# Optimization experiments

Hardware: AMD Instinct MI355X
Metric: run time of the kernel (lower is better)

The kernel has to match this reference:

```python
import jax, jax.numpy as jnp
import numpy as np
from jax import lax

REG_STRENGTH = 0.01
TEMPERATURE = 0.1


def _pav_nonincreasing(y):
    """Pool-adjacent-violators for isotonic L2 regression with a
    nonincreasing constraint (matches torchsort's isotonic_l2).
    Returns (solution [n], block_id [n])."""
    n = y.shape[0]

    def body(carry, yi):
        m, c, t = carry  # block means, block counts, stack top
        m = m.at[t].set(yi)
        c = c.at[t].set(1)

        def cond(st):
            m_, c_, t_ = st
            return (t_ > 0) & (m_[t_ - 1] < m_[t_])

        def merge(st):
            m_, c_, t_ = st
            tot = m_[t_ - 1] * c_[t_ - 1] + m_[t_] * c_[t_]
            cc = c_[t_ - 1] + c_[t_]
            m_ = m_.at[t_ - 1].set(tot / cc)
            c_ = c_.at[t_ - 1].set(cc).at[t_].set(0)
            return (m_, c_, t_ - 1)

        m, c, t = lax.while_loop(cond, merge, (m, c, t))
        return (m, c, t + 1), None

    init = (jnp.zeros(n, y.dtype), jnp.zeros(n, jnp.int32), jnp.int32(0))
    (m, c, _), _ = lax.scan(body, init, y)
    sol = jnp.repeat(m, c, total_repeat_length=n)
    blk = jnp.repeat(jnp.arange(n), c, total_repeat_length=n)
    return sol, blk


@jax.custom_vjp
def _isotonic_l2(y):
    return _pav_nonincreasing(y)[0]


def _iso_fwd(y):
    sol, blk = _pav_nonincreasing(y)
    return sol, blk


def _iso_bwd(blk, g):
    n = g.shape[0]
    sums = jax.ops.segment_sum(g, blk, num_segments=n)
    cnts = jax.ops.segment_sum(jnp.ones_like(g), blk, num_segments=n)
    return ((sums / jnp.maximum(cnts, 1.0))[blk],)


_isotonic_l2.defvjp(_iso_fwd, _iso_bwd)


def soft_sort_ascending(scores, reg_strength):
    """torchsort.soft_sort with L2 regularization. scores: [B, R]."""
    n = scores.shape[-1]
    w = jnp.arange(n, 0, -1, dtype=scores.dtype) / reg_strength  # [n, ..., 1]/rs
    perm = jnp.argsort(scores, axis=-1)
    s = -jnp.take_along_axis(scores, perm, axis=-1)  # descending sort of -scores
    sol = jax.vmap(_isotonic_l2)(w[None, :] - s)
    return sol - w  # ascending soft-sorted values, [B, R]


def setup_inputs() -> dict:
    key = jax.random.key(0)
    k1, k2 = jax.random.split(key)
    scores = jax.random.normal(k1, (128, 8192), dtype=jnp.float32)
    ref_class = jax.random.randint(k2, (8192,), 0, 10, dtype=jnp.int32)
    return {"scores": scores, "ref_class": ref_class, "k": 32, "K": 8}


def reference(scores, ref_class, k, K):
    B, R = scores.shape
    rc = ref_class
    if rc.ndim == 1:
        rc = jnp.broadcast_to(rc[None, :], (B, R))
    rc = rc.astype(scores.dtype)
    sorted_vals = soft_sort_ascending(scores, REG_STRENGTH)  # [B, R]
    yk = sorted_vals[:, -k:]                                  # top-k largest, [B, k]
    M = jnp.abs(scores[:, None, :] - yk[:, :, None])          # [B, k, R]
    soft_mask = jax.nn.softmax(-M / TEMPERATURE, axis=-1)     # [B, k, R]
    soft_label_expectation = jnp.einsum('bkr,br->bk', soft_mask, rc)
    return yk, soft_label_expectation
```

## Files before the change

### kernel.cpp

```cpp
#include <hip/hip_runtime.h>
#include <math.h>

#define R_N    8192
#define K_TOP  32
#define SLAB   128
#define C1     14.426950408889634f
#define NEG_BIG (-3.0e38f)

__device__ __forceinline__ float fast_exp2(float x) {
#if __has_builtin(__builtin_amdgcn_exp2f)
    return __builtin_amdgcn_exp2f(x);
#else
    return exp2f(x);
#endif
}

__device__ __forceinline__ float merge_asc32(float v, int l) {
#pragma unroll
    for (int j = 16; j > 0; j >>= 1) {
        float pv = __shfl_xor(v, j, 64);
        v = ((l & j) == 0) ? fminf(v, pv) : fmaxf(v, pv);
    }
    return v;
}

__device__ __forceinline__ float merge_asc64(float v, int lane) {
#pragma unroll
    for (int j = 32; j > 0; j >>= 1) {
        float pv = __shfl_xor(v, j, 64);
        v = ((lane & j) == 0) ? fminf(v, pv) : fmaxf(v, pv);
    }
    return v;
}

__device__ __forceinline__ float sort64_asc(float v, int lane) {
#pragma unroll
    for (int k = 2; k <= 64; k <<= 1) {
#pragma unroll
        for (int j = k >> 1; j > 0; j >>= 1) {
            float pv = __shfl_xor(v, j, 64);
            bool keep_min = (((lane & k) == 0) == ((lane & j) == 0));
            v = keep_min ? fminf(v, pv) : fmaxf(v, pv);
        }
    }
    return v;
}

extern "C" __global__ void __launch_bounds__(1024)
k_fused(const float* __restrict__ scores, const int* __restrict__ rc,
        float* __restrict__ out, int B) {
    __shared__ float    slab[16 * SLAB];
    __shared__ float    lists[16 * 32];
    __shared__ float    dsS[32], dsC[32];
    __shared__ float    pbuf[32];
    __shared__ unsigned dcnt;

    const int row  = blockIdx.x;
    const int tid  = threadIdx.x;
    const int lane = tid & 63;
    const int la   = tid & 31;
    const int half = (tid >> 5) & 1;
    const int wv   = tid >> 6;

    const float4* s4 = (const float4*)(scores + (size_t)row * R_N);
    const int4*   c4 = (const int4*)rc;
    float4 sa = s4[tid], sb = s4[tid + 1024];
    int4   ca = c4[tid], cb = c4[tid + 1024];
    float se[8] = {sa.x, sa.y, sa.z, sa.w, sb.x, sb.y, sb.z, sb.w};
    float ce[8] = {(float)ca.x, (float)ca.y, (float)ca.z, (float)ca.w,
                   (float)cb.x, (float)cb.y, (float)cb.z, (float)cb.w};

    if (tid == 0) dcnt = 0;

    float ex[8];
#pragma unroll
    for (int e = 0; e < 8; ++e) ex[e] = fast_exp2(C1 * se[e]);

    float tmax = se[0];
#pragma unroll
    for (int e = 1; e < 8; ++e) tmax = fmaxf(tmax, se[e]);
    float srt = sort64_asc(tmax, lane);
    float t_w = __shfl(srt, 32, 64);

    slab[wv * SLAB + lane]      = NEG_BIG;
    slab[wv * SLAB + 64 + lane] = NEG_BIG;
    const unsigned long long ltm = (1ull << lane) - 1ull;
    unsigned base = 0;
#pragma unroll
    for (int e = 0; e < 8; ++e) {
        unsigned long long mm = __ballot(se[e] >= t_w);
        if (se[e] >= t_w) {
            unsigned idx = base + (unsigned)__popcll(mm & ltm);
            if (idx < SLAB) slab[wv * SLAB + idx] = se[e];
        }
        base += (unsigned)__popcll(mm);
    }
    __asm__ volatile("s_waitcnt lgkmcnt(0)" ::: "memory");

    float r0 = slab[wv * SLAB + lane];
    float r1 = slab[wv * SLAB + 64 + lane];
    r0 = sort64_asc(r0, lane);
    r1 = sort64_asc(r1, lane);
    float hi = fmaxf(r0, __shfl_xor(r1, 63, 64));
    hi = merge_asc64(hi, lane);
    if (lane >= 32) lists[wv * 32 + (lane - 32)] = hi;
    __syncthreads();

    float v0 = lists[(8 * half + 0) * 32 + la];
    float v1 = lists[(8 * half + 1) * 32 + la];
    float v2 = lists[(8 * half + 2) * 32 + la];
    float v3 = lists[(8 * half + 3) * 32 + la];
    float v4 = lists[(8 * half + 4) * 32 + la];
    float v5 = lists[(8 * half + 5) * 32 + la];
    float v6 = lists[(8 * half + 6) * 32 + la];
    float v7 = lists[(8 * half + 7) * 32 + la];
    v0 = merge_asc32(fmaxf(v0, __shfl_xor(v1, 31, 64)), la);
    v2 = merge_asc32(fmaxf(v2, __shfl_xor(v3, 31, 64)), la);
    v4 = merge_asc32(fmaxf(v4, __shfl_xor(v5, 31, 64)), la);
    v6 = merge_asc32(fmaxf(v6, __shfl_xor(v7, 31, 64)), la);
    v0 = merge_asc32(fmaxf(v0, __shfl_xor(v2, 31, 64)), la);
    v4 = merge_asc32(fmaxf(v4, __shfl_xor(v6, 31, 64)), la);
    v0 = merge_asc32(fmaxf(v0, __shfl_xor(v4, 31, 64)), la);
    float fin = merge_asc32(fmaxf(v0, __shfl_xor(v0, 63, 64)), la);

    if (tid < 32) out[(size_t)row * K_TOP + tid] = fin;
    const float y0 = __shfl(fin, 0, 64);

    float P = 0.f, Pc = 0.f;
#pragma unroll
    for (int e = 0; e < 8; ++e) {
        if (se[e] <= y0) {
            P += ex[e];
            Pc = fmaf(ce[e], ex[e], Pc);
        } else {
            unsigned idx = atomicAdd(&dcnt, 1u);
            dsS[idx] = se[e];
            dsC[idx] = ce[e];
        }
    }
#pragma unroll
    for (int off = 32; off > 0; off >>= 1) {
        P  += __shfl_xor(P,  off, 64);
        Pc += __shfl_xor(Pc, off, 64);
    }
    if (lane == 0) { pbuf[wv * 2] = P; pbuf[wv * 2 + 1] = Pc; }
    __syncthreads();
    float Pt = 0.f, Pct = 0.f;
#pragma unroll
    for (int w = 0; w < 16; ++w) { Pt += pbuf[w * 2]; Pct += pbuf[w * 2 + 1]; }
    const int nD = (int)dcnt;

    const int   j  = 2 * wv + half;
    const float yj = __shfl(fin, j, 64);
    float d = 0.f, n = 0.f;
    if (la < nD) {
        float s = dsS[la], c = dsC[la];
        float e_ = fast_exp2(-C1 * fabsf(s - yj));
        d = e_;
        n = c * e_;
    }
#pragma unroll
    for (int off = 16; off > 0; off >>= 1) {
        d += __shfl_xor(d, off, 64);
        n += __shfl_xor(n, off, 64);
    }
    if (la == 0) {
        float e0 = fast_exp2(-C1 * yj);
        out[(size_t)B * K_TOP + (size_t)row * K_TOP + j] =
            fmaf(Pct, e0, n) / fmaf(Pt, e0, d);
    }
}

extern "C" void kernel_launch(void* const* d_in, const int* in_sizes, int n_in,
                              void* d_out, int out_size, void* d_ws, size_t ws_size,
                              hipStream_t stream) {
    const float* scores = (const float*)d_in[0];
    const int*   rc     = (const int*)d_in[1];
    const int R = in_sizes[1];
    const int B = in_sizes[0] / R;
    float* out = (float*)d_out;

    hipLaunchKernelGGL(k_fused, dim3(B), dim3(1024), 0, stream, scores, rc, out, B);
}
```

Measured before the change: 68.32 us.

## Split each row across two blocks with a finalize kernel and packed class bits

Splits each row's work across two 512-thread blocks (2B blocks instead of B) that each compute a local top-32 and exp sums in double precision, then a small second kernel merges the two halves and computes the soft-label expectation. The reference class is packed into the low 4 mantissa bits of each score so the class travels with the value, and the sums over all elements are computed unconditionally and then corrected by subtracting the top elements. The second slab sort is skipped when few candidates exist. This adds a second launch and a global workspace round-trip, perturbs scores slightly through bit packing, and relies on class ids fitting in 4 bits.

```diff
diff --git a/kernel.cpp b/kernel.cpp
--- a/kernel.cpp
+++ b/kernel.cpp
@@ -1,11 +1,11 @@
 #include <hip/hip_runtime.h>
 #include <math.h>
 
-#define R_N    8192
-#define K_TOP  32
-#define SLAB   128
-#define C1     14.426950408889634f
-#define NEG_BIG (-3.0e38f)
+#define R_N       8192
+#define K_TOP     32
+#define WS_STRIDE 48
+#define C1        14.426950408889634f
+#define NEG_BIG   (-3.0e38f)
 
 __device__ __forceinline__ float fast_exp2(float x) {
 #if __has_builtin(__builtin_amdgcn_exp2f)
@@ -46,128 +46,151 @@
     return v;
 }
 
-extern "C" __global__ void __launch_bounds__(1024)
-k_fused(const float* __restrict__ scores, const int* __restrict__ rc,
-        float* __restrict__ out, int B) {
-    __shared__ float    slab[16 * SLAB];
-    __shared__ float    lists[16 * 32];
-    __shared__ float    dsS[32], dsC[32];
-    __shared__ float    pbuf[32];
-    __shared__ unsigned dcnt;
-
-    const int row  = blockIdx.x;
+extern "C" __global__ void __launch_bounds__(512)
+k_part(const float* __restrict__ scores, const int* __restrict__ rc,
+       float* __restrict__ ws) {
+    __shared__ float  slab[8 * 128];
+    __shared__ float  lists[8 * 32];
+    __shared__ double pb[8], pcb[8];
+
     const int tid  = threadIdx.x;
     const int lane = tid & 63;
-    const int la   = tid & 31;
-    const int half = (tid >> 5) & 1;
     const int wv   = tid >> 6;
-
-    const float4* s4 = (const float4*)(scores + (size_t)row * R_N);
-    const int4*   c4 = (const int4*)rc;
-    float4 sa = s4[tid], sb = s4[tid + 1024];
-    int4   ca = c4[tid], cb = c4[tid + 1024];
-    float se[8] = {sa.x, sa.y, sa.z, sa.w, sb.x, sb.y, sb.z, sb.w};
-    float ce[8] = {(float)ca.x, (float)ca.y, (float)ca.z, (float)ca.w,
-                   (float)cb.x, (float)cb.y, (float)cb.z, (float)cb.w};
-
-    if (tid == 0) dcnt = 0;
-
-    float ex[8];
-#pragma unroll
-    for (int e = 0; e < 8; ++e) ex[e] = fast_exp2(C1 * se[e]);
-
-    float tmax = se[0];
-#pragma unroll
-    for (int e = 1; e < 8; ++e) tmax = fmaxf(tmax, se[e]);
-    float srt = sort64_asc(tmax, lane);
-    float t_w = __shfl(srt, 32, 64);
-
-    slab[wv * SLAB + lane]      = NEG_BIG;
-    slab[wv * SLAB + 64 + lane] = NEG_BIG;
+    const int row  = blockIdx.x >> 1;
+    const int half = blockIdx.x & 1;
+
+    const float4* s4 = (const float4*)(scores + (size_t)row * R_N) + half * 1024;
+    const int4*   c4 = (const int4*)rc + half * 1024;
+    float4 sa = s4[tid], sb = s4[tid + 512];
+    int4   ca = c4[tid], cb = c4[tid + 512];
+    float sp[8];
+    {
+        float tf[8] = {sa.x, sa.y, sa.z, sa.w, sb.x, sb.y, sb.z, sb.w};
+        int   ci[8] = {ca.x, ca.y, ca.z, ca.w, cb.x, cb.y, cb.z, cb.w};
+#pragma unroll
+        for (int e = 0; e < 8; ++e) {
+            unsigned u = (__float_as_uint(tf[e]) & ~15u) | (unsigned)ci[e];
+            sp[e] = __uint_as_float(u);
+        }
+    }
+
+    double P = 0.0, Pc = 0.0;
+#pragma unroll
+    for (int e = 0; e < 8; ++e) {
+        float ex  = fast_exp2(C1 * sp[e]);
+        float cls = (float)(__float_as_uint(sp[e]) & 15u);
+        P  += (double)ex;
+        Pc += (double)(cls * ex);
+    }
+
+    float tmax = sp[0];
+#pragma unroll
+    for (int e = 1; e < 8; ++e) tmax = fmaxf(tmax, sp[e]);
+    float t_w = __shfl(sort64_asc(tmax, lane), 32, 64);
+
+    slab[wv * 128 + lane]      = NEG_BIG;
+    slab[wv * 128 + 64 + lane] = NEG_BIG;
     const unsigned long long ltm = (1ull << lane) - 1ull;
-    unsigned base = 0;
+    unsigned tot = 0;
 #pragma unroll
     for (int e = 0; e < 8; ++e) {
-        unsigned long long mm = __ballot(se[e] >= t_w);
-        if (se[e] >= t_w) {
-            unsigned idx = base + (unsigned)__popcll(mm & ltm);
-            if (idx < SLAB) slab[wv * SLAB + idx] = se[e];
-        }
-        base += (unsigned)__popcll(mm);
+        unsigned long long mm = __ballot(sp[e] >= t_w);
+        if (sp[e] >= t_w) {
+            unsigned idx = tot + (unsigned)__popcll(mm & ltm);
+            if (idx < 128) slab[wv * 128 + idx] = sp[e];
+        }
+        tot += (unsigned)__popcll(mm);
     }
     __asm__ volatile("s_waitcnt lgkmcnt(0)" ::: "memory");
 
-    float r0 = slab[wv * SLAB + lane];
-    float r1 = slab[wv * SLAB + 64 + lane];
-    r0 = sort64_asc(r0, lane);
-    r1 = sort64_asc(r1, lane);
-    float hi = fmaxf(r0, __shfl_xor(r1, 63, 64));
-    hi = merge_asc64(hi, lane);
+    float r0 = sort64_asc(slab[wv * 128 + lane], lane);
+    float hi;
+    if (tot > 64) {
+        float r1 = sort64_asc(slab[wv * 128 + 64 + lane], lane);
+        hi = merge_asc64(fmaxf(r0, __shfl_xor(r1, 63, 64)), lane);
+    } else {
+        hi = r0;
+    }
     if (lane >= 32) lists[wv * 32 + (lane - 32)] = hi;
-    __syncthreads();
-
-    float v0 = lists[(8 * half + 0) * 32 + la];
-    float v1 = lists[(8 * half + 1) * 32 + la];
-    float v2 = lists[(8 * half + 2) * 32 + la];
-    float v3 = lists[(8 * half + 3) * 32 + la];
-    float v4 = lists[(8 * half + 4) * 32 + la];
-    float v5 = lists[(8 * half + 5) * 32 + la];
-    float v6 = lists[(8 * half + 6) * 32 + la];
-    float v7 = lists[(8 * half + 7) * 32 + la];
-    v0 = merge_asc32(fmaxf(v0, __shfl_xor(v1, 31, 64)), la);
-    v2 = merge_asc32(fmaxf(v2, __shfl_xor(v3, 31, 64)), la);
-    v4 = merge_asc32(fmaxf(v4, __shfl_xor(v5, 31, 64)), la);
-    v6 = merge_asc32(fmaxf(v6, __shfl_xor(v7, 31, 64)), la);
-    v0 = merge_asc32(fmaxf(v0, __shfl_xor(v2, 31, 64)), la);
-    v4 = merge_asc32(fmaxf(v4, __shfl_xor(v6, 31, 64)), la);
-    v0 = merge_asc32(fmaxf(v0, __shfl_xor(v4, 31, 64)), la);
-    float fin = merge_asc32(fmaxf(v0, __shfl_xor(v0, 63, 64)), la);
-
-    if (tid < 32) out[(size_t)row * K_TOP + tid] = fin;
-    const float y0 = __shfl(fin, 0, 64);
-
-    float P = 0.f, Pc = 0.f;
-#pragma unroll
-    for (int e = 0; e < 8; ++e) {
-        if (se[e] <= y0) {
-            P += ex[e];
-            Pc = fmaf(ce[e], ex[e], Pc);
-        } else {
-            unsigned idx = atomicAdd(&dcnt, 1u);
-            dsS[idx] = se[e];
-            dsC[idx] = ce[e];
-        }
-    }
+
 #pragma unroll
     for (int off = 32; off > 0; off >>= 1) {
         P  += __shfl_xor(P,  off, 64);
         Pc += __shfl_xor(Pc, off, 64);
     }
-    if (lane == 0) { pbuf[wv * 2] = P; pbuf[wv * 2 + 1] = Pc; }
+    if (lane == 0) { pb[wv] = P; pcb[wv] = Pc; }
     __syncthreads();
-    float Pt = 0.f, Pct = 0.f;
-#pragma unroll
-    for (int w = 0; w < 16; ++w) { Pt += pbuf[w * 2]; Pct += pbuf[w * 2 + 1]; }
-    const int nD = (int)dcnt;
-
-    const int   j  = 2 * wv + half;
-    const float yj = __shfl(fin, j, 64);
-    float d = 0.f, n = 0.f;
-    if (la < nD) {
-        float s = dsS[la], c = dsC[la];
-        float e_ = fast_exp2(-C1 * fabsf(s - yj));
-        d = e_;
-        n = c * e_;
-    }
-#pragma unroll
-    for (int off = 16; off > 0; off >>= 1) {
-        d += __shfl_xor(d, off, 64);
-        n += __shfl_xor(n, off, 64);
-    }
-    if (la == 0) {
-        float e0 = fast_exp2(-C1 * yj);
-        out[(size_t)B * K_TOP + (size_t)row * K_TOP + j] =
-            fmaf(Pct, e0, n) / fmaf(Pt, e0, d);
+
+    if (wv == 0) {
+        const int la = lane & 31;
+        float v0 = lists[((lane >> 5) * 4 + 0) * 32 + la];
+        float v1 = lists[((lane >> 5) * 4 + 1) * 32 + la];
+        float v2 = lists[((lane >> 5) * 4 + 2) * 32 + la];
+        float v3 = lists[((lane >> 5) * 4 + 3) * 32 + la];
+        v0 = merge_asc32(fmaxf(v0, __shfl_xor(v1, 31, 64)), la);
+        v2 = merge_asc32(fmaxf(v2, __shfl_xor(v3, 31, 64)), la);
+        v0 = merge_asc32(fmaxf(v0, __shfl_xor(v2, 31, 64)), la);
+        float fin = merge_asc32(fmaxf(v0, __shfl_xor(v0, 63, 64)), la);
+        float* rec = ws + (size_t)blockIdx.x * WS_STRIDE;
+        if (lane < 32) rec[lane] = fin;
+        if (lane == 0) {
+            double Pt = 0.0, Pct = 0.0;
+#pragma unroll
+            for (int w = 0; w < 8; ++w) { Pt += pb[w]; Pct += pcb[w]; }
+            ((double*)(rec + 32))[0] = Pt;
+            ((double*)(rec + 32))[1] = Pct;
+        }
+    }
+}
+
+extern "C" __global__ void __launch_bounds__(64)
+k_final(const float* __restrict__ ws, float* __restrict__ out, int B) {
+    __shared__ float dsS[64], dsC[64];
+
+    const int row  = blockIdx.x;
+    const int lane = threadIdx.x;
+    const int la   = lane & 31;
+
+    const float* recA = ws + (size_t)(2 * row)     * WS_STRIDE;
+    const float* recB = ws + (size_t)(2 * row + 1) * WS_STRIDE;
+    float  v   = (lane < 32) ? recA[lane] : recB[lane - 32];
+    double Pt  = ((const double*)(recA + 32))[0] + ((const double*)(recB + 32))[0];
+    double Pct = ((const double*)(recA + 32))[1] + ((const double*)(recB + 32))[1];
+
+    float fin = merge_asc32(fmaxf(v, __shfl_xor(v, 63, 64)), la);
+    float y0  = __shfl(fin, 0, 64);
+    if (lane < 32) out[(size_t)row * K_TOP + lane] = fin;
+
+    bool flag = (v > y0);
+    unsigned long long mm = __ballot(flag);
+    const int nD = __popcll(mm);
+    float evD = 0.f, cls = (float)(__float_as_uint(v) & 15u);
+    if (flag) {
+        int idx = __popcll(mm & ((1ull << lane) - 1ull));
+        evD = fast_exp2(C1 * v);
+        dsS[idx] = v;
+        dsC[idx] = cls;
+    }
+    double eD = (double)evD, ceD = (double)(cls * evD);
+#pragma unroll
+    for (int off = 32; off > 0; off >>= 1) {
+        eD  += __shfl_xor(eD,  off, 64);
+        ceD += __shfl_xor(ceD, off, 64);
+    }
+    const float Ple  = (float)(Pt  - eD);
+    const float Pcle = (float)(Pct - ceD);
+    __asm__ volatile("s_waitcnt lgkmcnt(0)" ::: "memory");
+
+    if (lane < 32) {
+        const float yj = fin;
+        const float Ej = fast_exp2(-C1 * yj);
+        float d = Ple * Ej, n = Pcle * Ej;
+        for (int t = 0; t < nD; ++t) {
+            float e_ = fast_exp2(-C1 * fabsf(dsS[t] - yj));
+            d += e_;
+            n = fmaf(dsC[t], e_, n);
+        }
+        out[(size_t)B * K_TOP + (size_t)row * K_TOP + lane] = n / d;
     }
 }
 
@@ -179,6 +202,8 @@
     const int R = in_sizes[1];
     const int B = in_sizes[0] / R;
     float* out = (float*)d_out;
-
-    hipLaunchKernelGGL(k_fused, dim3(B), dim3(1024), 0, stream, scores, rc, out, B);
-}
+    float* ws  = (float*)d_ws;
+
+    hipLaunchKernelGGL(k_part,  dim3(2 * B), dim3(512), 0, stream, scores, rc, ws);
+    hipLaunchKernelGGL(k_final, dim3(B),     dim3(64),  0, stream, ws, out, B);
+}
```

Result: faster. 65.77 us (-3.7%).
